# Kernel tuning notes

Hardware: AMD Instinct MI355X
Metric: run time of the kernel (lower is better)

Reference implementation:

```python
import math
import jax, jax.numpy as jnp
import numpy as np

N = 100000       # nodes
K = 32           # fixed neighbor fanout
D_IN = 128
D_OUT = 128
TPERC = 0.45


def setup_inputs() -> dict:
    key = jax.random.key(0)
    k1, k2, k3 = jax.random.split(key, 3)
    x = jax.random.normal(k1, (N, D_IN), dtype=jnp.float32)
    # nn.Linear weight [out, in], no bias
    W = jax.random.normal(k2, (D_OUT, D_IN), dtype=jnp.float32) * (1.0 / math.sqrt(D_IN))
    nbrs = jax.random.randint(k3, (N, K), 0, N, dtype=jnp.int32)
    return {"x": x, "W": W, "nbrs": nbrs}


def reference(x, W, nbrs):
    # h = Linear(x): [N, D_OUT]
    h = jnp.einsum("nd,od->no", x, W)
    # gather neighbor messages: [N, K, D_OUT]
    msgs = h[nbrs]
    # per-channel sort over the neighbor axis (matches torch.sort(dim=0) per node)
    msgs = jnp.sort(msgs, axis=1)
    remove = math.floor(K * TPERC)  # static: 14
    if remove > 0:
        msgs = msgs[:, remove:K - remove]
    # trimmed mean over remaining neighbors; activation is identity (None)
    return jnp.mean(msgs, axis=1)
```

## Files before the change

kernel.cpp:

```cpp
#include <hip/hip_runtime.h>
#include <hip/hip_fp16.h>

#define NN 100000
#define KK 32
#define DD 128

typedef _Float16 v8h __attribute__((ext_vector_type(8)));
typedef _Float16 v4h __attribute__((ext_vector_type(4)));
typedef _Float16 v2h __attribute__((ext_vector_type(2)));
typedef float    v4f __attribute__((ext_vector_type(4)));
typedef float    v2f __attribute__((ext_vector_type(2)));

#define LDH 136


__global__ __launch_bounds__(256)
void gemm_mfma_kernel(const float* __restrict__ x, const float* __restrict__ W,
                      _Float16* __restrict__ h) {
    __shared__ _Float16 w_lds[DD * LDH];
    __shared__ _Float16 x_lds[128 * LDH];

    const int tid = threadIdx.x;
    const int block_row = blockIdx.x * 128;

    {
        const float4* ws = (const float4*)W;
        #pragma unroll
        for (int t = 0; t < 16; ++t) {
            const int fi = tid + 256 * t;
            const int r = fi >> 5, c4 = fi & 31;
            const float4 f = ws[fi];
            v4h p = { (_Float16)f.x, (_Float16)f.y, (_Float16)f.z, (_Float16)f.w };
            *(v4h*)&w_lds[r * LDH + c4 * 4] = p;
        }
    }
    {
        const float4* xs = (const float4*)x;
        #pragma unroll
        for (int t = 0; t < 16; ++t) {
            const int fi = tid + 256 * t;
            const int r = fi >> 5, c4 = fi & 31;
            const int gr = block_row + r;
            float4 f = make_float4(0.f, 0.f, 0.f, 0.f);
            if (gr < NN) f = xs[(size_t)gr * 32 + c4];
            v4h p = { (_Float16)f.x, (_Float16)f.y, (_Float16)f.z, (_Float16)f.w };
            *(v4h*)&x_lds[r * LDH + c4 * 4] = p;
        }
    }
    __syncthreads();

    const int wv   = tid >> 6;
    const int lane = tid & 63;
    const int m    = lane & 15;
    const int quad = lane >> 4;

    const v4f zero = {0.f, 0.f, 0.f, 0.f};
    v4f acc[2][8];
    #pragma unroll
    for (int nt = 0; nt < 2; ++nt)
        #pragma unroll
        for (int ot = 0; ot < 8; ++ot) acc[nt][ot] = zero;

    #pragma unroll
    for (int ks = 0; ks < 4; ++ks) {
        const int kb = ks * 32 + quad * 8;
        const v8h xf0 = *(const v8h*)&x_lds[(wv * 32 + m) * LDH + kb];
        const v8h xf1 = *(const v8h*)&x_lds[(wv * 32 + 16 + m) * LDH + kb];
        #pragma unroll
        for (int ot = 0; ot < 8; ++ot) {
            const v8h wf = *(const v8h*)&w_lds[(ot * 16 + m) * LDH + kb];
            acc[0][ot] = __builtin_amdgcn_mfma_f32_16x16x32_f16(wf, xf0, acc[0][ot], 0, 0, 0);
            acc[1][ot] = __builtin_amdgcn_mfma_f32_16x16x32_f16(wf, xf1, acc[1][ot], 0, 0, 0);
        }
    }

    #pragma unroll
    for (int nt = 0; nt < 2; ++nt) {
        const int xr = block_row + wv * 32 + nt * 16 + m;
        if (xr < NN) {
            #pragma unroll
            for (int ot = 0; ot < 8; ++ot) {
                const v4f a = acc[nt][ot];
                v4h p = { (_Float16)a.x, (_Float16)a.y, (_Float16)a.z, (_Float16)a.w };
                const int c   = ot * 16 + quad * 4;
                const int s   = c >> 6;
                const int col = c & 63;
                *(v4h*)&h[((size_t)s * NN + xr) * 64 + col] = p;
            }
        }
    }
}

struct CEp { signed char a, b; };
struct Net16 { CEp ce[63]; };

constexpr int oem_merge(CEp* out, int c, int lo, int n, int r) {
    const int m = r * 2;
    if (m < n) {
        c = oem_merge(out, c, lo, n, m);
        c = oem_merge(out, c, lo + r, n, m);
        for (int i = lo + r; i + r < lo + n; i += m) {
            out[c].a = (signed char)i; out[c].b = (signed char)(i + r); ++c;
        }
    } else {
        out[c].a = (signed char)lo; out[c].b = (signed char)(lo + r); ++c;
    }
    return c;
}
constexpr int oem_sort(CEp* out, int c, int lo, int n) {
    if (n > 1) {
        const int m = n / 2;
        c = oem_sort(out, c, lo, m);
        c = oem_sort(out, c, lo + m, m);
        c = oem_merge(out, c, lo, n, 1);
    }
    return c;
}
constexpr Net16 make_net16() {
    Net16 net{};
    (void)oem_sort(net.ce, 0, 0, 16);
    return net;
}
constexpr Net16 NET16 = make_net16();

constexpr int WMAP(int i) { return i < 16 ? i : 47 - i; }

#define PKMIN(d, s0, s1) asm("v_pk_min_f16 %0, %1, %2" : "=v"(d) : "v"(s0), "v"(s1))
#define PKMAX(d, s0, s1) asm("v_pk_max_f16 %0, %1, %2" : "=v"(d) : "v"(s0), "v"(s1))

#define CEW(p, q) do {                                                  \
    v2h n_, x_;                                                         \
    PKMIN(n_, va[p], va[q]); PKMAX(x_, va[p], va[q]);                   \
    va[p] = n_; va[q] = x_; } while (0)

__global__ __launch_bounds__(256)
void trimmed_mean_kernel(const _Float16* __restrict__ h, const int* __restrict__ nbrs,
                         float* __restrict__ out) {
    __shared__ int s_nbr[8][33];

    const int tid      = threadIdx.x;
    const int slice    = blockIdx.x & 1;
    const int row_base = (blockIdx.x >> 1) * 8;

    s_nbr[tid >> 5][tid & 31] =
        __builtin_nontemporal_load(nbrs + (size_t)row_base * KK + tid);
    __syncthreads();

    const int q   = tid & 31;
    const int r   = tid >> 5;
    const int row = row_base + r;

    const char* base = (const char*)h + (size_t)slice * NN * 128;
    const unsigned int qoff = (unsigned int)q * 4u;

    v2h va[KK];
    #pragma unroll
    for (int k = 0; k < KK; ++k) {
        const unsigned int idx = (unsigned int)s_nbr[r][k];
        const unsigned int off = (idx << 7) | qoff;
        va[k] = __builtin_bit_cast(v2h, *(const unsigned int*)(base + off));
    }

    #pragma unroll
    for (int t = 0; t < 63; ++t) CEW(NET16.ce[t].a, NET16.ce[t].b);
    #pragma unroll
    for (int t = 0; t < 63; ++t) CEW(NET16.ce[t].a + 16, NET16.ce[t].b + 16);

    #pragma unroll
    for (int i = 0; i < 16; ++i) CEW(WMAP(i), WMAP(i + 16));
    #pragma unroll
    for (int i = 0; i < 8; ++i) { CEW(WMAP(i), WMAP(i + 8));
                                  CEW(WMAP(i + 16), WMAP(i + 24)); }
    #pragma unroll
    for (int i = 8; i < 12; ++i) { CEW(WMAP(i), WMAP(i + 4));
                                   CEW(WMAP(i + 8), WMAP(i + 12)); }
    CEW(WMAP(12), WMAP(14)); CEW(WMAP(13), WMAP(15));
    CEW(WMAP(16), WMAP(18)); CEW(WMAP(17), WMAP(19));

    v2f o;
    o.x = ((float)va[14].x + (float)va[15].x + (float)va[31].x + (float)va[30].x) * 0.25f;
    o.y = ((float)va[14].y + (float)va[15].y + (float)va[31].y + (float)va[30].y) * 0.25f;
    __builtin_nontemporal_store(
        o, (v2f*)(out + (size_t)row * DD + slice * 64) + q);
}

extern "C" void kernel_launch(void* const* d_in, const int* in_sizes, int n_in,
                              void* d_out, int out_size, void* d_ws, size_t ws_size,
                              hipStream_t stream) {
    const float* x    = (const float*)d_in[0];
    const float* W    = (const float*)d_in[1];
    const int*   nbrs = (const int*)d_in[2];
    float*       out  = (float*)d_out;
    _Float16*    h    = (_Float16*)d_ws;

    (void)in_sizes; (void)n_in; (void)out_size; (void)ws_size;

    gemm_mfma_kernel<<<(NN + 127) / 128, 256, 0, stream>>>(x, W, h);
    trimmed_mean_kernel<<<(NN / 8) * 2, 256, 0, stream>>>(h, nbrs, out);
}
```

Baseline: 206.0 us.

## Pre-sort neighbor indices into output buffer to improve gather locality

Adds a kernel that sorts each node's 32 neighbor indices with an odd-even merge network and writes two copies of them into the output buffer, one per channel slice. The trimmed-mean kernel then reads these sorted indices back from the output instead of the original neighbor array, and overwrites them with results. Sorting the indices makes each row's gathers run in ascending address order, which is meant to improve DRAM/cache access patterns. The cost is an extra kernel launch plus extra writes and reads of the index data, and the output buffer is reused as scratch space, which relies on each block reading its rows before any block writes them.

```diff
diff --git a/kernel.cpp b/kernel.cpp
--- a/kernel.cpp
+++ b/kernel.cpp
@@ -10,6 +10,7 @@
 typedef _Float16 v2h __attribute__((ext_vector_type(2)));
 typedef float    v4f __attribute__((ext_vector_type(4)));
 typedef float    v2f __attribute__((ext_vector_type(2)));
+typedef int      v4i __attribute__((ext_vector_type(4)));
 
 #define LDH 136
 
@@ -93,6 +94,7 @@
 
 struct CEp { signed char a, b; };
 struct Net16 { CEp ce[63]; };
+struct Net32 { CEp ce[191]; };
 
 constexpr int oem_merge(CEp* out, int c, int lo, int n, int r) {
     const int m = r * 2;
@@ -121,9 +123,46 @@
     (void)oem_sort(net.ce, 0, 0, 16);
     return net;
 }
+constexpr Net32 make_net32() {
+    Net32 net{};
+    (void)oem_sort(net.ce, 0, 0, 32);
+    return net;
+}
 constexpr Net16 NET16 = make_net16();
+constexpr Net32 NET32 = make_net32();
 
 constexpr int WMAP(int i) { return i < 16 ? i : 47 - i; }
+
+__global__ __launch_bounds__(256)
+void sort_nbrs_kernel(const int* __restrict__ nbrs, float* __restrict__ out) {
+    const int row = blockIdx.x * 256 + threadIdx.x;
+    if (row >= NN) return;
+
+    int v[KK];
+    const v4i* src = (const v4i*)(nbrs + (size_t)row * KK);
+    #pragma unroll
+    for (int t = 0; t < 8; ++t) {
+        const v4i u = __builtin_nontemporal_load(src + t);
+        v[t * 4 + 0] = u.x; v[t * 4 + 1] = u.y;
+        v[t * 4 + 2] = u.z; v[t * 4 + 3] = u.w;
+    }
+
+    #pragma unroll
+    for (int t = 0; t < 191; ++t) {
+        const int a = NET32.ce[t].a, b = NET32.ce[t].b;
+        const int lo = min(v[a], v[b]), hi = max(v[a], v[b]);
+        v[a] = lo; v[b] = hi;
+    }
+
+    int* dst = (int*)out + (size_t)row * DD;
+    #pragma unroll
+    for (int t = 0; t < 8; ++t) {
+        v4i u; u.x = v[t * 4]; u.y = v[t * 4 + 1];
+               u.z = v[t * 4 + 2]; u.w = v[t * 4 + 3];
+        *((v4i*)dst + t)        = u;
+        *((v4i*)(dst + 64) + t) = u;
+    }
+}
 
 #define PKMIN(d, s0, s1) asm("v_pk_min_f16 %0, %1, %2" : "=v"(d) : "v"(s0), "v"(s1))
 #define PKMAX(d, s0, s1) asm("v_pk_max_f16 %0, %1, %2" : "=v"(d) : "v"(s0), "v"(s1))
@@ -141,9 +180,13 @@
     const int tid      = threadIdx.x;
     const int slice    = blockIdx.x & 1;
     const int row_base = (blockIdx.x >> 1) * 8;
-
-    s_nbr[tid >> 5][tid & 31] =
-        __builtin_nontemporal_load(nbrs + (size_t)row_base * KK + tid);
+    (void)nbrs;
+
+    {
+        const int r = tid >> 5, c = tid & 31;
+        s_nbr[r][c] = __builtin_nontemporal_load(
+            (const int*)out + ((size_t)(row_base + r) * DD) + slice * 64 + c);
+    }
     __syncthreads();
 
     const int q   = tid & 31;
@@ -195,6 +238,7 @@
 
     (void)in_sizes; (void)n_in; (void)out_size; (void)ws_size;
 
+    sort_nbrs_kernel<<<(NN + 255) / 256, 256, 0, stream>>>(nbrs, out);
     gemm_mfma_kernel<<<(NN + 127) / 128, 256, 0, stream>>>(x, W, h);
     trimmed_mean_kernel<<<(NN / 8) * 2, 256, 0, stream>>>(h, nbrs, out);
 }
```

After: 224.2 us. +8.8%, slower.
